# Kernel tuning notes

Hardware: AMD Instinct MI355X
Metric: run time of the kernel (lower is better)

The kernel has to match this reference:

```python
import jax, jax.numpy as jnp
import numpy as np

N_HEAD = 16
ROPE_BASE = 10000.0


def setup_inputs() -> dict:
    key = jax.random.key(0)
    ks = jax.random.split(key, 5)
    B, T, C = 4, 1024, 2048
    s_in = 1.0 / np.sqrt(C)
    return {
        "x": jax.random.normal(ks[0], (B, T, C), dtype=jnp.float32),
        "w_attn": jax.random.normal(ks[1], (C, 3 * C), dtype=jnp.float32) * s_in,
        "b_attn": jax.random.normal(ks[2], (3 * C,), dtype=jnp.float32) * 0.01,
        "w_proj": jax.random.normal(ks[3], (C, C), dtype=jnp.float32) * s_in,
        "b_proj": jax.random.normal(ks[4], (C,), dtype=jnp.float32) * 0.01,
    }


def _rope(x, cos, sin):
    # x: (B, T, H, D); cos/sin: (T, D//2) -> broadcast over B, H
    d2 = x.shape[-1] // 2
    x1, x2 = x[..., :d2], x[..., d2:]
    c = cos[None, :, None, :]
    s = sin[None, :, None, :]
    return jnp.concatenate([x1 * c - x2 * s, x1 * s + x2 * c], axis=-1)


def reference(x, w_attn, b_attn, w_proj, b_proj):
    B, T, C = x.shape
    H = N_HEAD
    D = C // H
    qkv = (x @ w_attn + b_attn).reshape(B, T, 3, H, D)
    q, k, v = qkv[:, :, 0], qkv[:, :, 1], qkv[:, :, 2]  # (B, T, H, D)

    # Rotary embedding (GPT-NeoX / rotate-half style, full head dim)
    inv_freq = 1.0 / (ROPE_BASE ** (jnp.arange(0, D, 2, dtype=jnp.float32) / D))
    freqs = jnp.arange(T, dtype=jnp.float32)[:, None] * inv_freq[None, :]  # (T, D//2)
    cos, sin = jnp.cos(freqs), jnp.sin(freqs)
    q = _rope(q, cos, sin)
    k = _rope(k, cos, sin)

    scale = 1.0 / jnp.sqrt(jnp.asarray(D, dtype=x.dtype))
    att = jnp.einsum("bqhd,bkhd->bhqk", q, k) * scale  # (B, H, T, T)
    causal = jnp.tril(jnp.ones((T, T), dtype=bool))
    att = jnp.where(causal[None, None], att, jnp.asarray(-jnp.inf, dtype=att.dtype))
    att = jax.nn.softmax(att, axis=-1)
    y = jnp.einsum("bhqk,bkhd->bqhd", att, v).reshape(B, T, C)
    return y @ w_proj + b_proj
```

## Files before the change

kernel.cpp:

```cpp
#include <hip/hip_runtime.h>
#include <math.h>

#define T_SEQ 1024
#define C_DIM 2048
#define H_NUM 16
#define D_HEAD 128
#define BT 4096
#define QKV_N 6144

typedef __bf16 bf16x8 __attribute__((ext_vector_type(8)));
typedef float f32x4 __attribute__((ext_vector_type(4)));
typedef unsigned short u16;
typedef unsigned int u32;

#define AS1C(p) ((const __attribute__((address_space(1))) void*)(p))
#define AS3(p)  ((__attribute__((address_space(3))) void*)(p))

__device__ __forceinline__ u16 f2bf(float f) {
    u32 u = __builtin_bit_cast(u32, f);
    u += 0x7fffu + ((u >> 16) & 1u);
    return (u16)(u >> 16);
}
__device__ __forceinline__ void unpack8(uint4 u, float* f) {
    const u32 w0 = u.x, w1 = u.y, w2 = u.z, w3 = u.w;
    f[0] = __builtin_bit_cast(float, w0 << 16);
    f[1] = __builtin_bit_cast(float, w0 & 0xffff0000u);
    f[2] = __builtin_bit_cast(float, w1 << 16);
    f[3] = __builtin_bit_cast(float, w1 & 0xffff0000u);
    f[4] = __builtin_bit_cast(float, w2 << 16);
    f[5] = __builtin_bit_cast(float, w2 & 0xffff0000u);
    f[6] = __builtin_bit_cast(float, w3 << 16);
    f[7] = __builtin_bit_cast(float, w3 & 0xffff0000u);
}
__device__ __forceinline__ uint4 pack8(const float* f) {
    uint4 u;
    u.x = (u32)f2bf(f[0]) | ((u32)f2bf(f[1]) << 16);
    u.y = (u32)f2bf(f[2]) | ((u32)f2bf(f[3]) << 16);
    u.z = (u32)f2bf(f[4]) | ((u32)f2bf(f[5]) << 16);
    u.w = (u32)f2bf(f[6]) | ((u32)f2bf(f[7]) << 16);
    return u;
}

__global__ __launch_bounds__(256) void cast_bf16(
    const float* __restrict__ in, u16* __restrict__ out)
{
    int i = blockIdx.x * 256 + threadIdx.x;
    float4 v = ((const float4*)in)[i];
    ushort4 o;
    o.x = f2bf(v.x); o.y = f2bf(v.y); o.z = f2bf(v.z); o.w = f2bf(v.w);
    ((ushort4*)out)[i] = o;
}

__global__ __launch_bounds__(256) void transpose_cast(
    const float* __restrict__ in, u16* __restrict__ out, int R, int Cc)
{
    __shared__ float tile[32][33];
    const int c0 = blockIdx.x * 32, r0 = blockIdx.y * 32;
    const int tx = threadIdx.x & 31, ty = threadIdx.x >> 5;
#pragma unroll
    for (int i = 0; i < 32; i += 8)
        tile[ty + i][tx] = in[(size_t)(r0 + ty + i) * Cc + c0 + tx];
    __syncthreads();
#pragma unroll
    for (int i = 0; i < 32; i += 8)
        out[(size_t)(c0 + ty + i) * R + r0 + tx] = f2bf(tile[tx][ty + i]);
}

template <int OUT_BF16>
__global__ __launch_bounds__(512, 2) void gemm_bf16_192(
    const u16* __restrict__ A,
    const u16* __restrict__ Bt,
    const float* __restrict__ bias,
    void* __restrict__ Cout,
    int M, int N, int K)
{
    __shared__ alignas(16) char lds[2][57344];

    const int tid  = threadIdx.x;
    const int lane = tid & 63;
    const int w    = tid >> 6;
    const int wr   = w >> 2;
    const int wc   = w & 3;
    const int l15  = lane & 15;
    const int l4   = lane >> 4;
    const int m0   = blockIdx.y * 256;
    const int n0   = blockIdx.x * 192;
    const int NT   = K >> 6;

    f32x4 acc[8][3] = {};

    const int srow  = w * 16 + (lane >> 3);
    const int sslot = (lane & 7) ^ (lane >> 3);
    const size_t aoff = (size_t)(m0 + srow) * K + sslot * 8;
    const int brow_s = w * 8 + (lane >> 3);
    const size_t boff = (size_t)(n0 + brow_s) * K + sslot * 8;
    const int sdst = w * 2048;

    auto stageA = [&](char* buf, int h, int k0) {
#pragma unroll
        for (int i = 0; i < 2; ++i)
            __builtin_amdgcn_global_load_lds(
                AS1C(A + aoff + (size_t)(h * 128 + i * 8) * K + k0),
                AS3(buf + h * 16384 + sdst + i * 1024), 16, 0, 0);
    };
    auto stageB = [&](char* buf, int k0) {
#pragma unroll
        for (int i = 0; i < 3; ++i)
            __builtin_amdgcn_global_load_lds(
                AS1C(Bt + boff + (size_t)(i * 64) * K + k0),
                AS3(buf + 32768 + i * 8192 + w * 1024), 16, 0, 0);
    };

    stageB(lds[0], 0);
    stageA(lds[0], 0, 0);
    stageA(lds[0], 1, 0);
    stageB(lds[1], 64);
    stageA(lds[1], 0, 64);
    asm volatile("s_waitcnt vmcnt(5)" ::: "memory");
    __builtin_amdgcn_s_barrier();
    asm volatile("" ::: "memory");

    const int sl0  = (l4 ^ (l15 & 7)) << 4;
    const int sl1  = sl0 ^ 64;
    const int arow = (wr * 64 + l15) * 128;
    const int brow = 32768 + (wc * 48 + l15) * 128;

    for (int kt = 0; kt < NT; ++kt) {
        char* cb = lds[kt & 1];
        char* nb = lds[(kt & 1) ^ 1];

        bf16x8 bfr[3][2], af[4][2];
#pragma unroll
        for (int nt = 0; nt < 3; ++nt) {
            bfr[nt][0] = __builtin_bit_cast(bf16x8,
                *(const uint4*)(cb + brow + nt * 2048 + sl0));
            bfr[nt][1] = __builtin_bit_cast(bf16x8,
                *(const uint4*)(cb + brow + nt * 2048 + sl1));
        }
#pragma unroll
        for (int mt = 0; mt < 4; ++mt) {
            af[mt][0] = __builtin_bit_cast(bf16x8,
                *(const uint4*)(cb + arow + mt * 2048 + sl0));
            af[mt][1] = __builtin_bit_cast(bf16x8,
                *(const uint4*)(cb + arow + mt * 2048 + sl1));
        }
        if (kt + 1 < NT) stageA(nb, 1, (kt + 1) << 6);
        __builtin_amdgcn_s_setprio(1);
#pragma unroll
        for (int mt = 0; mt < 4; ++mt)
#pragma unroll
            for (int nt = 0; nt < 3; ++nt)
#pragma unroll
                for (int kk = 0; kk < 2; ++kk)
                    acc[mt][nt] = __builtin_amdgcn_mfma_f32_16x16x32_bf16(
                        af[mt][kk], bfr[nt][kk], acc[mt][nt], 0, 0, 0);
        __builtin_amdgcn_s_setprio(0);
        __builtin_amdgcn_s_barrier();
        asm volatile("" ::: "memory");

        bf16x8 ag[4][2];
#pragma unroll
        for (int mt = 0; mt < 4; ++mt) {
            ag[mt][0] = __builtin_bit_cast(bf16x8,
                *(const uint4*)(cb + 16384 + arow + mt * 2048 + sl0));
            ag[mt][1] = __builtin_bit_cast(bf16x8,
                *(const uint4*)(cb + 16384 + arow + mt * 2048 + sl1));
        }
        if (kt + 2 < NT) {
            stageB(cb, (kt + 2) << 6);
            stageA(cb, 0, (kt + 2) << 6);
        }
        __builtin_amdgcn_s_setprio(1);
#pragma unroll
        for (int mt = 0; mt < 4; ++mt)
#pragma unroll
            for (int nt = 0; nt < 3; ++nt)
#pragma unroll
                for (int kk = 0; kk < 2; ++kk)
                    acc[mt + 4][nt] = __builtin_amdgcn_mfma_f32_16x16x32_bf16(
                        ag[mt][kk], bfr[nt][kk], acc[mt + 4][nt], 0, 0, 0);
        __builtin_amdgcn_s_setprio(0);
        if (kt < NT - 2)
            asm volatile("s_waitcnt vmcnt(5)" ::: "memory");
        else
            asm volatile("s_waitcnt vmcnt(0)" ::: "memory");
        __builtin_amdgcn_s_barrier();
        asm volatile("" ::: "memory");
    }

#pragma unroll
    for (int nt = 0; nt < 3; ++nt) {
        const int colg = n0 + wc * 48 + nt * 16 + l15;
        const float bv = bias[colg];
#pragma unroll
        for (int mt = 0; mt < 8; ++mt) {
            const int rowb = m0 + ((mt >> 2) ? 128 : 0) + wr * 64
                           + (mt & 3) * 16 + l4 * 4;
#pragma unroll
            for (int r = 0; r < 4; ++r) {
                const float v = acc[mt][nt][r] + bv;
                if (OUT_BF16)
                    ((u16*)Cout)[(size_t)(rowb + r) * N + colg] = f2bf(v);
                else
                    ((float*)Cout)[(size_t)(rowb + r) * N + colg] = v;
            }
        }
    }
}

template <int OUT_BF16>
__global__ __launch_bounds__(512, 2) void gemm_bf16_256(
    const u16* __restrict__ A,
    const u16* __restrict__ Bt,
    const float* __restrict__ bias,
    void* __restrict__ Cout,
    int M, int N, int K)
{
    __shared__ alignas(16) char lds[2][49152];

    const int tid  = threadIdx.x;
    const int lane = tid & 63;
    const int w    = tid >> 6;
    const int wr   = w >> 1;
    const int wc   = w & 1;
    const int l15  = lane & 15;
    const int l4   = lane >> 4;
    const int m0   = blockIdx.y * 256;
    const int n0   = blockIdx.x * 128;
    const int NT   = K >> 6;

    f32x4 acc[4][4] = {};

    const int srow  = w * 16 + (lane >> 3);
    const int sslot = (lane & 7) ^ (lane >> 3);
    const size_t aoff = (size_t)(m0 + srow) * K + sslot * 8;
    const size_t boff = (size_t)(n0 + srow) * K + sslot * 8;
    const int sdst = w * 2048;

    auto stageA = [&](char* buf, int h, int k0) {
#pragma unroll
        for (int i = 0; i < 2; ++i)
            __builtin_amdgcn_global_load_lds(
                AS1C(A + aoff + (size_t)(h * 128 + i * 8) * K + k0),
                AS3(buf + h * 16384 + sdst + i * 1024), 16, 0, 0);
    };
    auto stageB = [&](char* buf, int k0) {
#pragma unroll
        for (int i = 0; i < 2; ++i)
            __builtin_amdgcn_global_load_lds(
                AS1C(Bt + boff + (size_t)(i * 8) * K + k0),
                AS3(buf + 32768 + sdst + i * 1024), 16, 0, 0);
    };

    stageB(lds[0], 0);
    stageA(lds[0], 0, 0);
    stageA(lds[0], 1, 0);
    stageB(lds[1], 64);
    stageA(lds[1], 0, 64);
    asm volatile("s_waitcnt vmcnt(4)" ::: "memory");
    __builtin_amdgcn_s_barrier();

    const int sl0  = (l4 ^ (l15 & 7)) << 4;
    const int sl1  = sl0 ^ 64;
    const int arow = (wr * 32 + l15) * 128;
    const int brow = 32768 + (wc * 64 + l15) * 128;

    for (int kt = 0; kt < NT; ++kt) {
        char* cb = lds[kt & 1];
        char* nb = lds[(kt & 1) ^ 1];

        bf16x8 bfr[4][2], af[2][2];
#pragma unroll
        for (int nt = 0; nt < 4; ++nt) {
            bfr[nt][0] = __builtin_bit_cast(bf16x8,
                *(const uint4*)(cb + brow + nt * 2048 + sl0));
            bfr[nt][1] = __builtin_bit_cast(bf16x8,
                *(const uint4*)(cb + brow + nt * 2048 + sl1));
        }
#pragma unroll
        for (int mt = 0; mt < 2; ++mt) {
            af[mt][0] = __builtin_bit_cast(bf16x8,
                *(const uint4*)(cb + arow + mt * 2048 + sl0));
            af[mt][1] = __builtin_bit_cast(bf16x8,
                *(const uint4*)(cb + arow + mt * 2048 + sl1));
        }
        if (kt + 1 < NT) stageA(nb, 1, (kt + 1) << 6);
        __builtin_amdgcn_s_barrier();
        asm volatile("s_waitcnt lgkmcnt(0)" ::: "memory");
        __builtin_amdgcn_s_setprio(1);
#pragma unroll
        for (int mt = 0; mt < 2; ++mt)
#pragma unroll
            for (int nt = 0; nt < 4; ++nt)
#pragma unroll
                for (int kk = 0; kk < 2; ++kk)
                    acc[mt][nt] = __builtin_amdgcn_mfma_f32_16x16x32_bf16(
                        af[mt][kk], bfr[nt][kk], acc[mt][nt], 0, 0, 0);
        __builtin_amdgcn_s_setprio(0);
        __builtin_amdgcn_s_barrier();

        bf16x8 ag[2][2];
#pragma unroll
        for (int mt = 0; mt < 2; ++mt) {
            ag[mt][0] = __builtin_bit_cast(bf16x8,
                *(const uint4*)(cb + 16384 + arow + mt * 2048 + sl0));
            ag[mt][1] = __builtin_bit_cast(bf16x8,
                *(const uint4*)(cb + 16384 + arow + mt * 2048 + sl1));
        }
        if (kt + 2 < NT) {
            stageB(cb, (kt + 2) << 6);
            stageA(cb, 0, (kt + 2) << 6);
        }
        __builtin_amdgcn_s_barrier();
        asm volatile("s_waitcnt lgkmcnt(0)" ::: "memory");
        __builtin_amdgcn_s_setprio(1);
#pragma unroll
        for (int mt = 0; mt < 2; ++mt)
#pragma unroll
            for (int nt = 0; nt < 4; ++nt)
#pragma unroll
                for (int kk = 0; kk < 2; ++kk)
                    acc[mt + 2][nt] = __builtin_amdgcn_mfma_f32_16x16x32_bf16(
                        ag[mt][kk], bfr[nt][kk], acc[mt + 2][nt], 0, 0, 0);
        __builtin_amdgcn_s_setprio(0);
        if (kt < NT - 2)
            asm volatile("s_waitcnt vmcnt(4)" ::: "memory");
        else
            asm volatile("s_waitcnt vmcnt(0)" ::: "memory");
        __builtin_amdgcn_s_barrier();
    }

#pragma unroll
    for (int nt = 0; nt < 4; ++nt) {
        const int colg = n0 + wc * 64 + nt * 16 + l15;
        const float bv = bias[colg];
#pragma unroll
        for (int mt = 0; mt < 4; ++mt) {
            const int rowb = m0 + (mt < 2 ? wr * 32 + mt * 16
                                          : 128 + wr * 32 + (mt - 2) * 16) + l4 * 4;
#pragma unroll
            for (int r = 0; r < 4; ++r) {
                const float v = acc[mt][nt][r] + bv;
                if (OUT_BF16)
                    ((u16*)Cout)[(size_t)(rowb + r) * N + colg] = f2bf(v);
                else
                    ((float*)Cout)[(size_t)(rowb + r) * N + colg] = v;
            }
        }
    }
}

__global__ __launch_bounds__(256) void rope_table(
    float* __restrict__ ct, float* __restrict__ st)
{
    const int i = blockIdx.x * 256 + threadIdx.x;
    const int d2 = i & 63, t = i >> 6;
    const float invf = expf(-(float)d2 * (9.210340371976184f / 64.0f));
    const float fr = (float)t * invf;
    ct[i] = cosf(fr);
    st[i] = sinf(fr);
}

__global__ __launch_bounds__(256) void rope_kv(
    const u16* __restrict__ qkv, const float* __restrict__ ct,
    const float* __restrict__ st,
    u16* __restrict__ Qc, u16* __restrict__ Kc, u16* __restrict__ Vt)
{
    const int tid = threadIdx.x;
    const int blk = blockIdx.x;
    const int tt = blk & 3;
    const int h  = (blk >> 2) & 15;
    const int b  = blk >> 6;
    const int t  = tt * 256 + tid;
    const int bh = b * 16 + h;

    const size_t src  = ((size_t)(b * T_SEQ + t)) * QKV_N + h * D_HEAD;
    const size_t dst  = ((size_t)(bh * T_SEQ + t)) * D_HEAD;
    const size_t vdst = ((size_t)bh * D_HEAD) * T_SEQ + t;
    const float* crow = ct + t * 64;
    const float* srow = st + t * 64;

#pragma unroll
    for (int part = 0; part < 2; ++part) {
        const u16* in  = qkv + src + part * C_DIM;
        u16* outp      = (part ? Kc : Qc) + dst;
#pragma unroll
        for (int c = 0; c < 8; ++c) {
            uint4 u1 = *(const uint4*)(in + c * 8);
            uint4 u2 = *(const uint4*)(in + 64 + c * 8);
            float f1[8], f2[8], o1[8], o2[8];
            unpack8(u1, f1); unpack8(u2, f2);
#pragma unroll
            for (int i = 0; i < 8; ++i) {
                const float cv = crow[c * 8 + i], sv = srow[c * 8 + i];
                o1[i] = f1[i] * cv - f2[i] * sv;
                o2[i] = f1[i] * sv + f2[i] * cv;
            }
            *(uint4*)(outp + c * 8)      = pack8(o1);
            *(uint4*)(outp + 64 + c * 8) = pack8(o2);
        }
    }

#pragma unroll
    for (int c = 0; c < 16; ++c) {
        uint4 v = *(const uint4*)(qkv + src + 2 * C_DIM + c * 8);
        u16 e[8];
        e[0] = (u16)(v.x & 0xffff); e[1] = (u16)(v.x >> 16);
        e[2] = (u16)(v.y & 0xffff); e[3] = (u16)(v.y >> 16);
        e[4] = (u16)(v.z & 0xffff); e[5] = (u16)(v.z >> 16);
        e[6] = (u16)(v.w & 0xffff); e[7] = (u16)(v.w >> 16);
#pragma unroll
        for (int j = 0; j < 8; ++j)
            Vt[vdst + (size_t)(c * 8 + j) * T_SEQ] = e[j];
    }
}

__global__ __launch_bounds__(256) void attn_mfma(
    const u16* __restrict__ Qc,
    const u16* __restrict__ Kc,
    const u16* __restrict__ Vt,
    u16* __restrict__ y)
{
    __shared__ alignas(16) char KsL[2][16384];
    __shared__ alignas(16) char VtsL[2][16384];
    __shared__ alignas(16) char PwL[4][2176];

    const int tid  = threadIdx.x;
    const int lane = tid & 63;
    const int w    = tid >> 6;
    const int l15  = lane & 15;
    const int l4   = lane >> 4;
    const int p    = blockIdx.x;
    const int bh   = blockIdx.y;
    const int h    = bh & 15;
    const int b    = bh >> 4;

    const size_t kbase = (size_t)bh * T_SEQ * D_HEAD;
    const size_t vbase = (size_t)bh * D_HEAD * T_SEQ;
    const float scale = 0.08838834764831845f;
    char* pw = PwL[w];

    for (int half = 0; half < 2; ++half) {
        const int qt = half ? (15 - p) : p;

        const int qrow = qt * 64 + w * 16 + l15;
        const u16* qptr = Qc + ((size_t)(bh * T_SEQ + qrow)) * D_HEAD;
        bf16x8 qf[4];
#pragma unroll
        for (int f = 0; f < 4; ++f)
            qf[f] = __builtin_bit_cast(bf16x8, *(const uint4*)(qptr + f * 32 + l4 * 8));

        f32x4 o[8] = {};
        float lrow[4] = {};

        __syncthreads();

        {
            const u16* ksrc = Kc + kbase + (size_t)(0 * 64 + lane) * D_HEAD;
#pragma unroll
            for (int i = 0; i < 4; ++i) {
                const int cd = w * 4 + i;
                __builtin_amdgcn_global_load_lds(AS1C(ksrc + cd * 8),
                                                 AS3(KsL[0] + cd * 1024), 16, 0, 0);
            }
#pragma unroll
            for (int i = 0; i < 4; ++i) {
                const int jc = w + (i >> 1) * 4;
                const int dh = i & 1;
                const u16* vsrc = Vt + vbase + (size_t)(dh * 64 + lane) * T_SEQ
                                  + 0 * 64 + jc * 8;
                __builtin_amdgcn_global_load_lds(AS1C(vsrc),
                                                 AS3(VtsL[0] + jc * 2048 + dh * 1024), 16, 0, 0);
            }
        }

        int buf = 0;
        for (int kt = 0; kt <= qt; ++kt, buf ^= 1) {
            __syncthreads();
            if (kt < qt) {
                const int kn = kt + 1;
                char* kb = KsL[buf ^ 1];
                char* vb = VtsL[buf ^ 1];
                const u16* ksrc = Kc + kbase + (size_t)(kn * 64 + lane) * D_HEAD;
#pragma unroll
                for (int i = 0; i < 4; ++i) {
                    const int cd = w * 4 + i;
                    __builtin_amdgcn_global_load_lds(AS1C(ksrc + cd * 8),
                                                     AS3(kb + cd * 1024), 16, 0, 0);
                }
#pragma unroll
                for (int i = 0; i < 4; ++i) {
                    const int jc = w + (i >> 1) * 4;
                    const int dh = i & 1;
                    const u16* vsrc = Vt + vbase + (size_t)(dh * 64 + lane) * T_SEQ
                                      + kn * 64 + jc * 8;
                    __builtin_amdgcn_global_load_lds(AS1C(vsrc),
                                                     AS3(vb + jc * 2048 + dh * 1024), 16, 0, 0);
                }
            }

            const char* kbuf = KsL[buf];
            const char* vbuf = VtsL[buf];

            f32x4 sacc[4] = {};
#pragma unroll
            for (int nb = 0; nb < 4; ++nb)
#pragma unroll
                for (int kc = 0; kc < 4; ++kc) {
                    bf16x8 kf = __builtin_bit_cast(bf16x8,
                        *(const uint4*)(kbuf + (kc * 4 + l4) * 1024 + (nb * 16 + l15) * 16));
                    sacc[nb] = __builtin_amdgcn_mfma_f32_16x16x32_bf16(
                        qf[kc], kf, sacc[nb], 0, 0, 0);
                }

#pragma unroll
            for (int nb = 0; nb < 4; ++nb)
#pragma unroll
                for (int r = 0; r < 4; ++r) {
                    const bool masked =
                        (kt == qt) && ((nb * 16 + l15) > (w * 16 + l4 * 4 + r));
                    const float e = masked ? 0.f
                        : __expf(sacc[nb][r] * scale - 8.0f);
                    sacc[nb][r] = e;
                    lrow[r] += e;
                }

#pragma unroll
            for (int nb = 0; nb < 4; ++nb)
#pragma unroll
                for (int r = 0; r < 4; ++r) {
                    const int j = nb * 16 + l15;
                    const int q = l4 * 4 + r;
                    *(u16*)(pw + (j >> 3) * 272 + q * 16 + (j & 7) * 2) =
                        f2bf(sacc[nb][r]);
                }

            bf16x8 pf[2];
#pragma unroll
            for (int kc2 = 0; kc2 < 2; ++kc2)
                pf[kc2] = __builtin_bit_cast(bf16x8,
                    *(const uint4*)(pw + (kc2 * 4 + l4) * 272 + l15 * 16));
#pragma unroll
            for (int db = 0; db < 8; ++db)
#pragma unroll
                for (int kc2 = 0; kc2 < 2; ++kc2) {
                    bf16x8 vf = __builtin_bit_cast(bf16x8,
                        *(const uint4*)(vbuf + (kc2 * 4 + l4) * 2048 + (db * 16 + l15) * 16));
                    o[db] = __builtin_amdgcn_mfma_f32_16x16x32_bf16(
                        pf[kc2], vf, o[db], 0, 0, 0);
                }
        }

        float inv[4];
#pragma unroll
        for (int r = 0; r < 4; ++r) {
            float ls = lrow[r];
#pragma unroll
            for (int off = 1; off < 16; off <<= 1)
                ls += __shfl_xor(ls, off, 64);
            inv[r] = 1.f / ls;
        }
#pragma unroll
        for (int db = 0; db < 8; ++db)
#pragma unroll
            for (int r = 0; r < 4; ++r) {
                const int q = qt * 64 + w * 16 + l4 * 4 + r;
                const int d = h * D_HEAD + db * 16 + l15;
                y[(size_t)(b * T_SEQ + q) * C_DIM + d] = f2bf(o[db][r] * inv[r]);
            }
    }
}

extern "C" void kernel_launch(void* const* d_in, const int* in_sizes, int n_in,
                              void* d_out, int out_size, void* d_ws, size_t ws_size,
                              hipStream_t stream) {
    const float* x      = (const float*)d_in[0];
    const float* w_attn = (const float*)d_in[1];
    const float* b_attn = (const float*)d_in[2];
    const float* w_proj = (const float*)d_in[3];
    const float* b_proj = (const float*)d_in[4];
    float* out = (float*)d_out;

    char* ws = (char*)d_ws;
    u16* xb   = (u16*)(ws);
    u16* waT  = (u16*)(ws + 16777216);
    u16* Qc   = (u16*)(ws);
    u16* Kc   = (u16*)(ws + 16777216);
    u16* Vt   = (u16*)(ws + 33554432);
    u16* qkvb = (u16*)(ws + 50331648);
    u16* wpT  = (u16*)(ws + 50331648);
    u16* yb   = (u16*)(ws + 100663296);
    float* ct = (float*)(ws + 100663296);
    float* st = ct + 65536;

    cast_bf16<<<(BT * C_DIM / 4) / 256, 256, 0, stream>>>(x, xb);
    transpose_cast<<<dim3(QKV_N / 32, C_DIM / 32), 256, 0, stream>>>(w_attn, waT, C_DIM, QKV_N);
    rope_table<<<(T_SEQ * 64) / 256, 256, 0, stream>>>(ct, st);

    gemm_bf16_192<1><<<dim3(QKV_N / 192, BT / 256), 512, 0, stream>>>(
        xb, waT, b_attn, qkvb, BT, QKV_N, C_DIM);

    rope_kv<<<256, 256, 0, stream>>>(qkvb, ct, st, Qc, Kc, Vt);

    transpose_cast<<<dim3(C_DIM / 32, C_DIM / 32), 256, 0, stream>>>(w_proj, wpT, C_DIM, C_DIM);

    attn_mfma<<<dim3(8, 4 * H_NUM), 256, 0, stream>>>(Qc, Kc, Vt, yb);

    gemm_bf16_256<0><<<dim3(C_DIM / 128, BT / 256), 512, 0, stream>>>(
        yb, wpT, b_proj, out, BT, C_DIM, C_DIM);
}
```

Measured before the change: 386.8 us.

## Coalesce RoPE/V-transpose kernel via LDS tile and trim GEMM barriers

The rope_kv kernel is restructured so that 16 lanes cooperatively load one row of Q/K, using a lane shuffle to fetch the rotate-half partner. V is transposed through a shared-memory tile, so the 2-byte scattered global stores become coalesced 16-byte row writes. In the GEMM main loop, the barrier and lgkmcnt wait between the LDS fragment reads and the MFMA block are removed, and the remaining barriers get compiler memory fences. This leaves the compiler's own waitcnt insertion to order the LDS reads. The aim is to cut uncoalesced memory traffic and synchronisation stalls, at the cost of extra LDS use and relying on the implicit buffer ordering for correctness.

```diff
diff --git a/kernel.cpp b/kernel.cpp
--- a/kernel.cpp
+++ b/kernel.cpp
@@ -41,6 +41,12 @@
     return u;
 }
 
+__device__ __forceinline__ void ph_barrier() {
+    asm volatile("" ::: "memory");
+    __builtin_amdgcn_s_barrier();
+    asm volatile("" ::: "memory");
+}
+
 __global__ __launch_bounds__(256) void cast_bf16(
     const float* __restrict__ in, u16* __restrict__ out)
 {
@@ -258,7 +264,7 @@
     stageB(lds[1], 64);
     stageA(lds[1], 0, 64);
     asm volatile("s_waitcnt vmcnt(4)" ::: "memory");
-    __builtin_amdgcn_s_barrier();
+    ph_barrier();
 
     const int sl0  = (l4 ^ (l15 & 7)) << 4;
     const int sl1  = sl0 ^ 64;
@@ -285,8 +291,6 @@
                 *(const uint4*)(cb + arow + mt * 2048 + sl1));
         }
         if (kt + 1 < NT) stageA(nb, 1, (kt + 1) << 6);
-        __builtin_amdgcn_s_barrier();
-        asm volatile("s_waitcnt lgkmcnt(0)" ::: "memory");
         __builtin_amdgcn_s_setprio(1);
 #pragma unroll
         for (int mt = 0; mt < 2; ++mt)
@@ -297,7 +301,7 @@
                     acc[mt][nt] = __builtin_amdgcn_mfma_f32_16x16x32_bf16(
                         af[mt][kk], bfr[nt][kk], acc[mt][nt], 0, 0, 0);
         __builtin_amdgcn_s_setprio(0);
-        __builtin_amdgcn_s_barrier();
+        ph_barrier();
 
         bf16x8 ag[2][2];
 #pragma unroll
@@ -311,8 +315,6 @@
             stageB(cb, (kt + 2) << 6);
             stageA(cb, 0, (kt + 2) << 6);
         }
-        __builtin_amdgcn_s_barrier();
-        asm volatile("s_waitcnt lgkmcnt(0)" ::: "memory");
         __builtin_amdgcn_s_setprio(1);
 #pragma unroll
         for (int mt = 0; mt < 2; ++mt)
@@ -327,7 +329,7 @@
             asm volatile("s_waitcnt vmcnt(4)" ::: "memory");
         else
             asm volatile("s_waitcnt vmcnt(0)" ::: "memory");
-        __builtin_amdgcn_s_barrier();
+        ph_barrier();
     }
 
 #pragma unroll
@@ -366,44 +368,56 @@
     const float* __restrict__ st,
     u16* __restrict__ Qc, u16* __restrict__ Kc, u16* __restrict__ Vt)
 {
+    __shared__ u16 vtile[128][264];
     const int tid = threadIdx.x;
     const int blk = blockIdx.x;
     const int tt = blk & 3;
     const int h  = (blk >> 2) & 15;
     const int b  = blk >> 6;
-    const int t  = tt * 256 + tid;
     const int bh = b * 16 + h;
 
-    const size_t src  = ((size_t)(b * T_SEQ + t)) * QKV_N + h * D_HEAD;
-    const size_t dst  = ((size_t)(bh * T_SEQ + t)) * D_HEAD;
-    const size_t vdst = ((size_t)bh * D_HEAD) * T_SEQ + t;
-    const float* crow = ct + t * 64;
-    const float* srow = st + t * 64;
-
-#pragma unroll
-    for (int part = 0; part < 2; ++part) {
-        const u16* in  = qkv + src + part * C_DIM;
-        u16* outp      = (part ? Kc : Qc) + dst;
-#pragma unroll
-        for (int c = 0; c < 8; ++c) {
-            uint4 u1 = *(const uint4*)(in + c * 8);
-            uint4 u2 = *(const uint4*)(in + 64 + c * 8);
-            float f1[8], f2[8], o1[8], o2[8];
-            unpack8(u1, f1); unpack8(u2, f2);
-#pragma unroll
-            for (int i = 0; i < 8; ++i) {
-                const float cv = crow[c * 8 + i], sv = srow[c * 8 + i];
-                o1[i] = f1[i] * cv - f2[i] * sv;
-                o2[i] = f1[i] * sv + f2[i] * cv;
-            }
-            *(uint4*)(outp + c * 8)      = pack8(o1);
-            *(uint4*)(outp + 64 + c * 8) = pack8(o2);
-        }
-    }
-
+    const int c8 = tid & 15;
+    const int rg = tid >> 4;
+    const float sgn = (c8 < 8) ? -1.f : 1.f;
+
+#pragma unroll 4
+    for (int s = 0; s < 16; ++s) {
+        const int row = s * 16 + rg;
+        const int t   = tt * 256 + row;
+        const size_t rsrc = (size_t)(b * T_SEQ + t) * QKV_N + h * D_HEAD;
+        const size_t rdst = (size_t)(bh * T_SEQ + t) * D_HEAD + c8 * 8;
+
+        const float* crow = ct + t * 64 + (c8 & 7) * 8;
+        const float* srow = st + t * 64 + (c8 & 7) * 8;
+        float cs[8], sn[8];
+        *(float4*)(cs)     = *(const float4*)(crow);
+        *(float4*)(cs + 4) = *(const float4*)(crow + 4);
+        *(float4*)(sn)     = *(const float4*)(srow);
+        *(float4*)(sn + 4) = *(const float4*)(srow + 4);
+
+#pragma unroll
+        for (int part = 0; part < 2; ++part) {
+            uint4 u = *(const uint4*)(qkv + rsrc + part * C_DIM + c8 * 8);
+            uint4 pu;
+            pu.x = (u32)__shfl_xor((int)u.x, 8, 64);
+            pu.y = (u32)__shfl_xor((int)u.y, 8, 64);
+            pu.z = (u32)__shfl_xor((int)u.z, 8, 64);
+            pu.w = (u32)__shfl_xor((int)u.w, 8, 64);
+            float f[8], pf[8], o[8];
+            unpack8(u, f); unpack8(pu, pf);
+#pragma unroll
+            for (int i = 0; i < 8; ++i)
+                o[i] = f[i] * cs[i] + sgn * pf[i] * sn[i];
+            u16* outp = (part ? Kc : Qc) + rdst;
+            *(uint4*)outp = pack8(o);
+        }
+    }
+
+    const int t = tt * 256 + tid;
+    const size_t vsrc = (size_t)(b * T_SEQ + t) * QKV_N + 2 * C_DIM + h * D_HEAD;
 #pragma unroll
     for (int c = 0; c < 16; ++c) {
-        uint4 v = *(const uint4*)(qkv + src + 2 * C_DIM + c * 8);
+        uint4 v = *(const uint4*)(qkv + vsrc + c * 8);
         u16 e[8];
         e[0] = (u16)(v.x & 0xffff); e[1] = (u16)(v.x >> 16);
         e[2] = (u16)(v.y & 0xffff); e[3] = (u16)(v.y >> 16);
@@ -411,7 +425,17 @@
         e[6] = (u16)(v.w & 0xffff); e[7] = (u16)(v.w >> 16);
 #pragma unroll
         for (int j = 0; j < 8; ++j)
-            Vt[vdst + (size_t)(c * 8 + j) * T_SEQ] = e[j];
+            vtile[c * 8 + j][tid] = e[j];
+    }
+    __syncthreads();
+
+    const int dl = tid >> 5;
+    const int jc = (tid & 31) * 8;
+    u16* vt = Vt + ((size_t)bh * D_HEAD) * T_SEQ + (size_t)tt * 256;
+#pragma unroll
+    for (int pass = 0; pass < 16; ++pass) {
+        const int d = pass * 8 + dl;
+        *(uint4*)(vt + (size_t)d * T_SEQ + jc) = *(const uint4*)&vtile[d][jc];
     }
 }
 
```

Result: faster. 362.6 us (-6.2%).
